# Performance work log

Measured on AMD Instinct MI355X. Metric: run time of the kernel, lower is better.

Reference implementation:

```python
import jax, jax.numpy as jnp
import numpy as np

EPS = 1e-10
BETA_SCALE = 1.0
TEMP = 0.5


def setup_inputs() -> dict:
    key = jax.random.key(0)
    ks = jax.random.split(key, 8)
    D = 128
    return {
        "root_mu_min": jax.random.normal(ks[0], (1, 64, D), dtype=jnp.float32),
        "root_mu_max": jax.random.normal(ks[1], (1, 64, D), dtype=jnp.float32),
        "root_beta_min_raw": jax.random.normal(ks[2], (1, 64, D), dtype=jnp.float32),
        "root_beta_max_raw": jax.random.normal(ks[3], (1, 64, D), dtype=jnp.float32),
        "adj_logits0": jax.random.normal(ks[4], (512, 64), dtype=jnp.float32),
        "adj_logits1": jax.random.normal(ks[5], (2048, 512), dtype=jnp.float32),
        "u0": jax.random.uniform(ks[6], (1, 512, 64), dtype=jnp.float32),
        "u1": jax.random.uniform(ks[7], (1, 2048, 512), dtype=jnp.float32),
    }


def _gumbel_sigmoid_hard(logits, u):
    # gumbel noise from externally supplied uniforms, straight-through hard threshold
    g = -jnp.log(-jnp.log(u + EPS) + EPS)
    y_soft = jax.nn.sigmoid((logits + g) / TEMP)
    y_hard = (y_soft > 0.5).astype(y_soft.dtype)
    return y_hard - jax.lax.stop_gradient(y_soft) + y_soft


def _weighted_intersection(mu_min, mu_max, beta_min, beta_max, w):
    # w: (1, C, P); parent boxes: (1, P, D)
    wsum = jnp.sum(w, axis=2)[..., None] + EPS                      # (1, C, 1)
    b_min = jnp.einsum('bcp,bpd->bcd', w, beta_min) / wsum           # (1, C, D)
    b_max = jnp.einsum('bcp,bpd->bcd', w, beta_max) / wsum           # (1, C, D)
    logw = jnp.log(w + EPS)[..., None]                               # (1, C, P, 1)
    arg_min = logw + mu_min[:, None, :, :] / b_min[:, :, None, :]    # (1, C, P, D)
    mu_min_i = b_min * jax.nn.logsumexp(arg_min, axis=2)             # (1, C, D)
    arg_max = logw - mu_max[:, None, :, :] / b_max[:, :, None, :]    # (1, C, P, D)
    mu_max_i = -b_max * jax.nn.logsumexp(arg_max, axis=2)            # (1, C, D)
    return mu_min_i, mu_max_i, b_min, b_max


def reference(root_mu_min, root_mu_max, root_beta_min_raw, root_beta_max_raw,
              adj_logits0, adj_logits1, u0, u1):
    beta_min = jax.nn.sigmoid(root_beta_min_raw) * BETA_SCALE + 1e-6
    beta_max = jax.nn.sigmoid(root_beta_max_raw) * BETA_SCALE + 1e-6
    level = (root_mu_min, root_mu_max, beta_min, beta_max)
    outs = list(level)
    for logits, u in ((adj_logits0, u0), (adj_logits1, u1)):
        w = _gumbel_sigmoid_hard(logits[None], u)  # (1, C, P)
        level = _weighted_intersection(*level, w)
        outs.extend(level)
    return tuple(outs)
```

## Files before the change

### kernel.cpp

```cpp
#include <hip/hip_runtime.h>
#include <cmath>

#define DD 128
#define LOG2E 1.4426950408889634f

__device__ __forceinline__ float sigm(float x) { return 1.0f / (1.0f + __expf(-x)); }

__device__ __forceinline__ unsigned fenc(float f) {
    unsigned b = __float_as_uint(f);
    return (b & 0x80000000u) ? ~b : (b | 0x80000000u);
}
__device__ __forceinline__ float fdec(unsigned e) {
    return (e & 0x80000000u) ? __uint_as_float(e ^ 0x80000000u) : __uint_as_float(~e);
}

__global__ void k_root(const float* __restrict__ mu_min, const float* __restrict__ mu_max,
                       const float* __restrict__ braw_min, const float* __restrict__ braw_max,
                       float* __restrict__ out, unsigned* __restrict__ cm_enc) {
    int i = blockIdx.x * 256 + threadIdx.x;
    out[i] = mu_min[i];
    out[8192 + i] = mu_max[i];
    out[16384 + i] = sigm(braw_min[i]) + 1e-6f;
    out[24576 + i] = sigm(braw_max[i]) + 1e-6f;
    if (blockIdx.x == 0) {
        cm_enc[threadIdx.x] = 0u;
        cm_enc[threadIdx.x + 256] = 0u;
    }
}

template<int P, int RPB>
__global__ __launch_bounds__(512)
void k_packprep(const float* __restrict__ mu_min, const float* __restrict__ mu_max,
                const float* __restrict__ b_min, const float* __restrict__ b_max,
                float2* __restrict__ mu2, float2* __restrict__ bb2,
                unsigned* __restrict__ e_min, unsigned* __restrict__ e_neg) {
    __shared__ float s1[4][DD], s2[4][DD];
    const int d = threadIdx.x & (DD - 1);
    const int rg = threadIdx.x >> 7;
    const int r0 = blockIdx.x * RPB;
    float m1 = -INFINITY, m2 = -INFINITY;
    for (int r = rg; r < RPB; r += 4) {
        int i = (r0 + r) * DD + d;
        float a = mu_min[i], b = mu_max[i];
        mu2[i] = make_float2(a, b);
        bb2[i] = make_float2(b_min[i], b_max[i]);
        m1 = fmaxf(m1, a);
        m2 = fmaxf(m2, -b);
    }
    s1[rg][d] = m1; s2[rg][d] = m2;
    __syncthreads();
    if (threadIdx.x < DD) {
        float a = fmaxf(fmaxf(s1[0][d], s1[1][d]), fmaxf(s1[2][d], s1[3][d]));
        float b = fmaxf(fmaxf(s2[0][d], s2[1][d]), fmaxf(s2[2][d], s2[3][d]));
        atomicMax(e_min + d, fenc(a));
        atomicMax(e_neg + d, fenc(b));
        if (blockIdx.x == 0) {
            mu2[P * DD + d] = make_float2(-1e38f, 1e38f);
            bb2[P * DD + d] = make_float2(0.0f, 0.0f);
        }
    }
}

template<int P, int NWAVE>
__global__ __launch_bounds__(NWAVE * 64, 4)
void k_levelw(const float* __restrict__ logits, const float* __restrict__ u,
              const float2* __restrict__ bb2, const float2* __restrict__ mu2,
              const unsigned* __restrict__ e_min, const unsigned* __restrict__ e_neg,
              float* __restrict__ o_mu_min, float* __restrict__ o_mu_max,
              float* __restrict__ o_b_min, float* __restrict__ o_b_max) {
    __shared__ __align__(16) int plist[NWAVE * P];
    const int tid = threadIdx.x;
    const int w = tid >> 6;
    const int lane = tid & 63;
    const int c = blockIdx.x * NWAVE + w;
    int* pl = &plist[w * P];

    int base = 0;
    #pragma unroll
    for (int it = 0; it < P / 64; ++it) {
        int p = it * 64 + lane;
        int idx = c * P + p;
        float uu = u[idx] + 1e-10f;
        float g = -__logf(-__logf(uu) + 1e-10f);
        bool pres = (logits[idx] + g) > 0.0f;
        unsigned long long m = __ballot(pres);
        if (pres) {
            int pos = __popcll(m & ((1ull << lane) - 1));
            pl[base + pos] = p << 10;
        }
        base += (int)__popcll(m);
    }
    const int n = base;
    int npad = (n + 7) & ~7;
    if (npad == 0) npad = 8;
    if (lane < npad - n) pl[n + lane] = P << 10;

    const unsigned lb = (unsigned)(lane << 4);
    const char* bbc = (const char*)bb2;
    const char* muc = (const char*)mu2;
    const int T = npad >> 3;

    float dmn0 = 0.f, dmx0 = 0.f, dmn1 = 0.f, dmx1 = 0.f;
    for (int k = 0; k < npad; k += 8) {
        int4 A = *(const int4*)(pl + k);
        int4 B = *(const int4*)(pl + k + 4);
        float4 r0 = *(const float4*)(bbc + ((unsigned)A.x + lb));
        float4 r1 = *(const float4*)(bbc + ((unsigned)A.y + lb));
        float4 r2 = *(const float4*)(bbc + ((unsigned)A.z + lb));
        float4 r3 = *(const float4*)(bbc + ((unsigned)A.w + lb));
        float4 r4 = *(const float4*)(bbc + ((unsigned)B.x + lb));
        float4 r5 = *(const float4*)(bbc + ((unsigned)B.y + lb));
        float4 r6 = *(const float4*)(bbc + ((unsigned)B.z + lb));
        float4 r7 = *(const float4*)(bbc + ((unsigned)B.w + lb));
        dmn0 += (r0.x + r1.x) + (r2.x + r3.x) + (r4.x + r5.x) + (r6.x + r7.x);
        dmx0 += (r0.y + r1.y) + (r2.y + r3.y) + (r4.y + r5.y) + (r6.y + r7.y);
        dmn1 += (r0.z + r1.z) + (r2.z + r3.z) + (r4.z + r5.z) + (r6.z + r7.z);
        dmx1 += (r0.w + r1.w) + (r2.w + r3.w) + (r4.w + r5.w) + (r6.w + r7.w);
    }

    const float wsv = (float)n + 1e-10f;
    const float bmin0 = dmn0 / wsv, bmax0 = dmx0 / wsv;
    const float bmin1 = dmn1 / wsv, bmax1 = dmx1 / wsv;
    const float rmin0 = 1.0f / fmaxf(bmin0, 1e-30f);
    const float rmin1 = 1.0f / fmaxf(bmin1, 1e-30f);
    const float nrmax0 = -1.0f / fmaxf(bmax0, 1e-30f);
    const float nrmax1 = -1.0f / fmaxf(bmax1, 1e-30f);
    uint2 em = *(const uint2*)(e_min + 2 * lane);
    uint2 en = *(const uint2*)(e_neg + 2 * lane);
    const float Mm0 = fdec(em.x), Mm1 = fdec(em.y);
    const float Mg0 = fdec(en.x), Mg1 = fdec(en.y);
    const float rm20 = rmin0 * LOG2E, rm21 = rmin1 * LOG2E;
    const float nx20 = nrmax0 * LOG2E, nx21 = nrmax1 * LOG2E;
    const float nM10 = -rm20 * Mm0, nM11 = -rm21 * Mm1;
    const float nM20 = nx20 * Mg0, nM21 = nx21 * Mg1;

    float s10 = 0.f, s20 = 0.f, s11 = 0.f, s21 = 0.f;
    {
        float4 q[8];
        {
            int4 A = *(const int4*)(pl);
            int4 B = *(const int4*)(pl + 4);
            q[0] = *(const float4*)(muc + ((unsigned)A.x + lb));
            q[1] = *(const float4*)(muc + ((unsigned)A.y + lb));
            q[2] = *(const float4*)(muc + ((unsigned)A.z + lb));
            q[3] = *(const float4*)(muc + ((unsigned)A.w + lb));
            q[4] = *(const float4*)(muc + ((unsigned)B.x + lb));
            q[5] = *(const float4*)(muc + ((unsigned)B.y + lb));
            q[6] = *(const float4*)(muc + ((unsigned)B.z + lb));
            q[7] = *(const float4*)(muc + ((unsigned)B.w + lb));
        }
        int k = 0;
        for (int t = 1; t < T; ++t) {
            k += 8;
            int4 A = *(const int4*)(pl + k);
            int4 B = *(const int4*)(pl + k + 4);
            float4 qn[8];
            qn[0] = *(const float4*)(muc + ((unsigned)A.x + lb));
            qn[1] = *(const float4*)(muc + ((unsigned)A.y + lb));
            qn[2] = *(const float4*)(muc + ((unsigned)A.z + lb));
            qn[3] = *(const float4*)(muc + ((unsigned)A.w + lb));
            qn[4] = *(const float4*)(muc + ((unsigned)B.x + lb));
            qn[5] = *(const float4*)(muc + ((unsigned)B.y + lb));
            qn[6] = *(const float4*)(muc + ((unsigned)B.z + lb));
            qn[7] = *(const float4*)(muc + ((unsigned)B.w + lb));
            #pragma unroll
            for (int z = 0; z < 8; ++z) {
                s10 += __builtin_amdgcn_exp2f(fmaf(q[z].x, rm20, nM10));
                s20 += __builtin_amdgcn_exp2f(fmaf(q[z].y, nx20, nM20));
                s11 += __builtin_amdgcn_exp2f(fmaf(q[z].z, rm21, nM11));
                s21 += __builtin_amdgcn_exp2f(fmaf(q[z].w, nx21, nM21));
            }
            #pragma unroll
            for (int z = 0; z < 8; ++z) q[z] = qn[z];
        }
        #pragma unroll
        for (int z = 0; z < 8; ++z) {
            s10 += __builtin_amdgcn_exp2f(fmaf(q[z].x, rm20, nM10));
            s20 += __builtin_amdgcn_exp2f(fmaf(q[z].y, nx20, nM20));
            s11 += __builtin_amdgcn_exp2f(fmaf(q[z].z, rm21, nM11));
            s21 += __builtin_amdgcn_exp2f(fmaf(q[z].w, nx21, nM21));
        }
    }

    const int idx = c * DD + 2 * lane;
    float v10 = bmin0 * fmaf(rmin0, Mm0, __logf(fmaxf(s10, 1e-35f)));
    float v11 = bmin1 * fmaf(rmin1, Mm1, __logf(fmaxf(s11, 1e-35f)));
    float v20 = -bmax0 * fmaf(-nrmax0, Mg0, __logf(fmaxf(s20, 1e-35f)));
    float v21 = -bmax1 * fmaf(-nrmax1, Mg1, __logf(fmaxf(s21, 1e-35f)));
    *(float2*)(o_mu_min + idx) = make_float2(v10, v11);
    *(float2*)(o_mu_max + idx) = make_float2(v20, v21);
    *(float2*)(o_b_min + idx)  = make_float2(bmin0, bmin1);
    *(float2*)(o_b_max + idx)  = make_float2(bmax0, bmax1);
}

extern "C" void kernel_launch(void* const* d_in, const int* in_sizes, int n_in,
                              void* d_out, int out_size, void* d_ws, size_t ws_size,
                              hipStream_t stream) {
    const float* mu_min0  = (const float*)d_in[0];
    const float* mu_max0  = (const float*)d_in[1];
    const float* braw_min = (const float*)d_in[2];
    const float* braw_max = (const float*)d_in[3];
    const float* adj0     = (const float*)d_in[4];
    const float* adj1     = (const float*)d_in[5];
    const float* u0       = (const float*)d_in[6];
    const float* u1       = (const float*)d_in[7];
    float* out = (float*)d_out;
    float* ws = (float*)d_ws;

    unsigned* cm_enc = (unsigned*)ws;
    unsigned* cm0_min = cm_enc;
    unsigned* cm0_neg = cm_enc + 128;
    unsigned* cm1_min = cm_enc + 256;
    unsigned* cm1_neg = cm_enc + 384;
    float2* mu2_0 = (float2*)(ws + 512);
    float2* bb2_0 = mu2_0 + 65 * DD;
    float2* mu2_1 = bb2_0 + 65 * DD;
    float2* bb2_1 = mu2_1 + 513 * DD;


    k_root<<<dim3(32), dim3(256), 0, stream>>>(mu_min0, mu_max0, braw_min, braw_max,
                                               out, cm_enc);

    k_packprep<64, 8><<<dim3(8), dim3(512), 0, stream>>>(
        mu_min0, mu_max0, out + 16384, out + 24576, mu2_0, bb2_0, cm0_min, cm0_neg);

    k_levelw<64, 2><<<dim3(256), dim3(128), 0, stream>>>(
        adj0, u0, bb2_0, mu2_0, cm0_min, cm0_neg,
        out + 32768, out + 98304, out + 163840, out + 229376);

    k_packprep<512, 8><<<dim3(64), dim3(512), 0, stream>>>(
        out + 32768, out + 98304, out + 163840, out + 229376, mu2_1, bb2_1, cm1_min, cm1_neg);

    k_levelw<512, 4><<<dim3(512), dim3(256), 0, stream>>>(
        adj1, u1, bb2_1, mu2_1, cm1_min, cm1_neg,
        out + 294912, out + 557056, out + 819200, out + 1081344);
}
```

Baseline: 133.2 us.

## Split each child's parent list across two waves and fuse root with pack prep

Each child is now handled by two waves. Each wave takes alternating 8-parent chunks of the shared parent list, and the partial beta sums and partial exp sums are combined through LDS with block barriers. This doubles the number of waves for level 1 and halves each wave's serial gather chain. The beta-sum loop also gains the same register prefetch used in the exp loop. Separately, the root sigmoid kernel and the level-0 pack/max prep are fused into one kernel, with a memset zeroing the atomic max buffers instead. The cost is redundant Gumbel/ballot work in both waves, identical duplicate writes to the parent list, and extra barriers.

```diff
diff --git a/kernel.cpp b/kernel.cpp
--- a/kernel.cpp
+++ b/kernel.cpp
@@ -14,17 +14,32 @@
     return (e & 0x80000000u) ? __uint_as_float(e ^ 0x80000000u) : __uint_as_float(~e);
 }
 
-__global__ void k_root(const float* __restrict__ mu_min, const float* __restrict__ mu_max,
-                       const float* __restrict__ braw_min, const float* __restrict__ braw_max,
-                       float* __restrict__ out, unsigned* __restrict__ cm_enc) {
-    int i = blockIdx.x * 256 + threadIdx.x;
-    out[i] = mu_min[i];
-    out[8192 + i] = mu_max[i];
-    out[16384 + i] = sigm(braw_min[i]) + 1e-6f;
-    out[24576 + i] = sigm(braw_max[i]) + 1e-6f;
-    if (blockIdx.x == 0) {
-        cm_enc[threadIdx.x] = 0u;
-        cm_enc[threadIdx.x + 256] = 0u;
+__global__ __launch_bounds__(512)
+void k_root0(const float* __restrict__ mu_min, const float* __restrict__ mu_max,
+             const float* __restrict__ braw_min, const float* __restrict__ braw_max,
+             float* __restrict__ out,
+             float2* __restrict__ mu2_0, float2* __restrict__ bb2_0,
+             unsigned* __restrict__ e_min0, unsigned* __restrict__ e_neg0) {
+    __shared__ float r1[4][DD], r2[4][DD];
+    const int i = blockIdx.x * 512 + threadIdx.x;
+    const int rg = threadIdx.x >> 7, d = threadIdx.x & (DD - 1);
+    float mn = mu_min[i], mx = mu_max[i];
+    float bm = sigm(braw_min[i]) + 1e-6f;
+    float bx = sigm(braw_max[i]) + 1e-6f;
+    out[i] = mn; out[8192 + i] = mx; out[16384 + i] = bm; out[24576 + i] = bx;
+    mu2_0[i] = make_float2(mn, mx);
+    bb2_0[i] = make_float2(bm, bx);
+    r1[rg][d] = mn; r2[rg][d] = -mx;
+    __syncthreads();
+    if (threadIdx.x < DD) {
+        float a = fmaxf(fmaxf(r1[0][d], r1[1][d]), fmaxf(r1[2][d], r1[3][d]));
+        float b = fmaxf(fmaxf(r2[0][d], r2[1][d]), fmaxf(r2[2][d], r2[3][d]));
+        atomicMax(e_min0 + d, fenc(a));
+        atomicMax(e_neg0 + d, fenc(b));
+        if (blockIdx.x == 0) {
+            mu2_0[64 * DD + d] = make_float2(-1e38f, 1e38f);
+            bb2_0[64 * DD + d] = make_float2(0.0f, 0.0f);
+        }
     }
 }
 
@@ -61,19 +76,21 @@
     }
 }
 
-template<int P, int NWAVE>
-__global__ __launch_bounds__(NWAVE * 64, 4)
+template<int P>
+__global__ __launch_bounds__(256, 4)
 void k_levelw(const float* __restrict__ logits, const float* __restrict__ u,
               const float2* __restrict__ bb2, const float2* __restrict__ mu2,
               const unsigned* __restrict__ e_min, const unsigned* __restrict__ e_neg,
               float* __restrict__ o_mu_min, float* __restrict__ o_mu_max,
               float* __restrict__ o_b_min, float* __restrict__ o_b_max) {
-    __shared__ __align__(16) int plist[NWAVE * P];
+    __shared__ __align__(16) int plist[2][P];
+    __shared__ float4 red[2][2][64];
     const int tid = threadIdx.x;
     const int w = tid >> 6;
     const int lane = tid & 63;
-    const int c = blockIdx.x * NWAVE + w;
-    int* pl = &plist[w * P];
+    const int j = w >> 1, h = w & 1;
+    const int c = blockIdx.x * 2 + j;
+    int* pl = plist[j];
 
     int base = 0;
     #pragma unroll
@@ -91,36 +108,66 @@
         base += (int)__popcll(m);
     }
     const int n = base;
-    int npad = (n + 7) & ~7;
-    if (npad == 0) npad = 8;
+    int npad = (n + 15) & ~15;
+    if (npad == 0) npad = 16;
     if (lane < npad - n) pl[n + lane] = P << 10;
 
     const unsigned lb = (unsigned)(lane << 4);
     const char* bbc = (const char*)bb2;
     const char* muc = (const char*)mu2;
-    const int T = npad >> 3;
+    const int Th = npad >> 4;
 
     float dmn0 = 0.f, dmx0 = 0.f, dmn1 = 0.f, dmx1 = 0.f;
-    for (int k = 0; k < npad; k += 8) {
-        int4 A = *(const int4*)(pl + k);
-        int4 B = *(const int4*)(pl + k + 4);
-        float4 r0 = *(const float4*)(bbc + ((unsigned)A.x + lb));
-        float4 r1 = *(const float4*)(bbc + ((unsigned)A.y + lb));
-        float4 r2 = *(const float4*)(bbc + ((unsigned)A.z + lb));
-        float4 r3 = *(const float4*)(bbc + ((unsigned)A.w + lb));
-        float4 r4 = *(const float4*)(bbc + ((unsigned)B.x + lb));
-        float4 r5 = *(const float4*)(bbc + ((unsigned)B.y + lb));
-        float4 r6 = *(const float4*)(bbc + ((unsigned)B.z + lb));
-        float4 r7 = *(const float4*)(bbc + ((unsigned)B.w + lb));
-        dmn0 += (r0.x + r1.x) + (r2.x + r3.x) + (r4.x + r5.x) + (r6.x + r7.x);
-        dmx0 += (r0.y + r1.y) + (r2.y + r3.y) + (r4.y + r5.y) + (r6.y + r7.y);
-        dmn1 += (r0.z + r1.z) + (r2.z + r3.z) + (r4.z + r5.z) + (r6.z + r7.z);
-        dmx1 += (r0.w + r1.w) + (r2.w + r3.w) + (r4.w + r5.w) + (r6.w + r7.w);
-    }
-
+    {
+        float4 q[8];
+        int k = h * 8;
+        {
+            int4 A = *(const int4*)(pl + k);
+            int4 B = *(const int4*)(pl + k + 4);
+            q[0] = *(const float4*)(bbc + ((unsigned)A.x + lb));
+            q[1] = *(const float4*)(bbc + ((unsigned)A.y + lb));
+            q[2] = *(const float4*)(bbc + ((unsigned)A.z + lb));
+            q[3] = *(const float4*)(bbc + ((unsigned)A.w + lb));
+            q[4] = *(const float4*)(bbc + ((unsigned)B.x + lb));
+            q[5] = *(const float4*)(bbc + ((unsigned)B.y + lb));
+            q[6] = *(const float4*)(bbc + ((unsigned)B.z + lb));
+            q[7] = *(const float4*)(bbc + ((unsigned)B.w + lb));
+        }
+        for (int t = 1; t < Th; ++t) {
+            k += 16;
+            int4 A = *(const int4*)(pl + k);
+            int4 B = *(const int4*)(pl + k + 4);
+            float4 qn[8];
+            qn[0] = *(const float4*)(bbc + ((unsigned)A.x + lb));
+            qn[1] = *(const float4*)(bbc + ((unsigned)A.y + lb));
+            qn[2] = *(const float4*)(bbc + ((unsigned)A.z + lb));
+            qn[3] = *(const float4*)(bbc + ((unsigned)A.w + lb));
+            qn[4] = *(const float4*)(bbc + ((unsigned)B.x + lb));
+            qn[5] = *(const float4*)(bbc + ((unsigned)B.y + lb));
+            qn[6] = *(const float4*)(bbc + ((unsigned)B.z + lb));
+            qn[7] = *(const float4*)(bbc + ((unsigned)B.w + lb));
+            dmn0 += (q[0].x + q[1].x) + (q[2].x + q[3].x) + (q[4].x + q[5].x) + (q[6].x + q[7].x);
+            dmx0 += (q[0].y + q[1].y) + (q[2].y + q[3].y) + (q[4].y + q[5].y) + (q[6].y + q[7].y);
+            dmn1 += (q[0].z + q[1].z) + (q[2].z + q[3].z) + (q[4].z + q[5].z) + (q[6].z + q[7].z);
+            dmx1 += (q[0].w + q[1].w) + (q[2].w + q[3].w) + (q[4].w + q[5].w) + (q[6].w + q[7].w);
+            #pragma unroll
+            for (int z = 0; z < 8; ++z) q[z] = qn[z];
+        }
+        dmn0 += (q[0].x + q[1].x) + (q[2].x + q[3].x) + (q[4].x + q[5].x) + (q[6].x + q[7].x);
+        dmx0 += (q[0].y + q[1].y) + (q[2].y + q[3].y) + (q[4].y + q[5].y) + (q[6].y + q[7].y);
+        dmn1 += (q[0].z + q[1].z) + (q[2].z + q[3].z) + (q[4].z + q[5].z) + (q[6].z + q[7].z);
+        dmx1 += (q[0].w + q[1].w) + (q[2].w + q[3].w) + (q[4].w + q[5].w) + (q[6].w + q[7].w);
+    }
+    red[j][h][lane] = make_float4(dmn0, dmx0, dmn1, dmx1);
+    __syncthreads();
+
+    float4 pb0 = red[j][0][lane];
+    float4 pb1 = red[j][1][lane];
     const float wsv = (float)n + 1e-10f;
-    const float bmin0 = dmn0 / wsv, bmax0 = dmx0 / wsv;
-    const float bmin1 = dmn1 / wsv, bmax1 = dmx1 / wsv;
+    const float bmin0 = (pb0.x + pb1.x) / wsv;
+    const float bmax0 = (pb0.y + pb1.y) / wsv;
+    const float bmin1 = (pb0.z + pb1.z) / wsv;
+    const float bmax1 = (pb0.w + pb1.w) / wsv;
     const float rmin0 = 1.0f / fmaxf(bmin0, 1e-30f);
     const float rmin1 = 1.0f / fmaxf(bmin1, 1e-30f);
     const float nrmax0 = -1.0f / fmaxf(bmax0, 1e-30f);
@@ -133,13 +180,15 @@
     const float nx20 = nrmax0 * LOG2E, nx21 = nrmax1 * LOG2E;
     const float nM10 = -rm20 * Mm0, nM11 = -rm21 * Mm1;
     const float nM20 = nx20 * Mg0, nM21 = nx21 * Mg1;
+    __syncthreads();
 
     float s10 = 0.f, s20 = 0.f, s11 = 0.f, s21 = 0.f;
     {
         float4 q[8];
+        int k = h * 8;
         {
-            int4 A = *(const int4*)(pl);
-            int4 B = *(const int4*)(pl + 4);
+            int4 A = *(const int4*)(pl + k);
+            int4 B = *(const int4*)(pl + k + 4);
             q[0] = *(const float4*)(muc + ((unsigned)A.x + lb));
             q[1] = *(const float4*)(muc + ((unsigned)A.y + lb));
             q[2] = *(const float4*)(muc + ((unsigned)A.z + lb));
@@ -149,9 +198,8 @@
             q[6] = *(const float4*)(muc + ((unsigned)B.z + lb));
             q[7] = *(const float4*)(muc + ((unsigned)B.w + lb));
         }
-        int k = 0;
-        for (int t = 1; t < T; ++t) {
-            k += 8;
+        for (int t = 1; t < Th; ++t) {
+            k += 16;
             int4 A = *(const int4*)(pl + k);
             int4 B = *(const int4*)(pl + k + 4);
             float4 qn[8];
@@ -181,16 +229,26 @@
             s21 += __builtin_amdgcn_exp2f(fmaf(q[z].w, nx21, nM21));
         }
     }
-
-    const int idx = c * DD + 2 * lane;
-    float v10 = bmin0 * fmaf(rmin0, Mm0, __logf(fmaxf(s10, 1e-35f)));
-    float v11 = bmin1 * fmaf(rmin1, Mm1, __logf(fmaxf(s11, 1e-35f)));
-    float v20 = -bmax0 * fmaf(-nrmax0, Mg0, __logf(fmaxf(s20, 1e-35f)));
-    float v21 = -bmax1 * fmaf(-nrmax1, Mg1, __logf(fmaxf(s21, 1e-35f)));
-    *(float2*)(o_mu_min + idx) = make_float2(v10, v11);
-    *(float2*)(o_mu_max + idx) = make_float2(v20, v21);
-    *(float2*)(o_b_min + idx)  = make_float2(bmin0, bmin1);
-    *(float2*)(o_b_max + idx)  = make_float2(bmax0, bmax1);
+    red[j][h][lane] = make_float4(s10, s20, s11, s21);
+    __syncthreads();
+
+    if (h == 0) {
+        float4 pc0 = red[j][0][lane];
+        float4 pc1 = red[j][1][lane];
+        const float S10 = fmaxf(pc0.x + pc1.x, 1e-35f);
+        const float S20 = fmaxf(pc0.y + pc1.y, 1e-35f);
+        const float S11 = fmaxf(pc0.z + pc1.z, 1e-35f);
+        const float S21 = fmaxf(pc0.w + pc1.w, 1e-35f);
+        const int idx = c * DD + 2 * lane;
+        float v10 = bmin0 * fmaf(rmin0, Mm0, __logf(S10));
+        float v11 = bmin1 * fmaf(rmin1, Mm1, __logf(S11));
+        float v20 = -bmax0 * fmaf(-nrmax0, Mg0, __logf(S20));
+        float v21 = -bmax1 * fmaf(-nrmax1, Mg1, __logf(S21));
+        *(float2*)(o_mu_min + idx) = make_float2(v10, v11);
+        *(float2*)(o_mu_max + idx) = make_float2(v20, v21);
+        *(float2*)(o_b_min + idx)  = make_float2(bmin0, bmin1);
+        *(float2*)(o_b_max + idx)  = make_float2(bmax0, bmax1);
+    }
 }
 
 extern "C" void kernel_launch(void* const* d_in, const int* in_sizes, int n_in,
@@ -207,7 +265,7 @@
     float* out = (float*)d_out;
     float* ws = (float*)d_ws;
 
-    unsigned* cm_enc = (unsigned*)ws;
+    unsigned* cm_enc  = (unsigned*)ws;
     unsigned* cm0_min = cm_enc;
     unsigned* cm0_neg = cm_enc + 128;
     unsigned* cm1_min = cm_enc + 256;
@@ -218,20 +276,19 @@
     float2* bb2_1 = mu2_1 + 513 * DD;
 
 
-    k_root<<<dim3(32), dim3(256), 0, stream>>>(mu_min0, mu_max0, braw_min, braw_max,
-                                               out, cm_enc);
-
-    k_packprep<64, 8><<<dim3(8), dim3(512), 0, stream>>>(
-        mu_min0, mu_max0, out + 16384, out + 24576, mu2_0, bb2_0, cm0_min, cm0_neg);
-
-    k_levelw<64, 2><<<dim3(256), dim3(128), 0, stream>>>(
+    hipMemsetAsync(cm_enc, 0, 512 * sizeof(unsigned), stream);
+
+    k_root0<<<dim3(16), dim3(512), 0, stream>>>(
+        mu_min0, mu_max0, braw_min, braw_max, out, mu2_0, bb2_0, cm0_min, cm0_neg);
+
+    k_levelw<64><<<dim3(256), dim3(256), 0, stream>>>(
         adj0, u0, bb2_0, mu2_0, cm0_min, cm0_neg,
         out + 32768, out + 98304, out + 163840, out + 229376);
 
     k_packprep<512, 8><<<dim3(64), dim3(512), 0, stream>>>(
         out + 32768, out + 98304, out + 163840, out + 229376, mu2_1, bb2_1, cm1_min, cm1_neg);
 
-    k_levelw<512, 4><<<dim3(512), dim3(256), 0, stream>>>(
+    k_levelw<512><<<dim3(1024), dim3(256), 0, stream>>>(
         adj1, u1, bb2_1, mu2_1, cm1_min, cm1_neg,
         out + 294912, out + 557056, out + 819200, out + 1081344);
 }
```

After: 132.1 us. No clear change (-0.8%).
